# Optimization experiments

Hardware: AMD Instinct MI355X
Metric: run time of the kernel (lower is better)

## Reference

```python
import jax, jax.numpy as jnp
import numpy as np

B, N, F_IN, H, L, C = 64, 512, 21, 64, 3, 9
NEG_INF = -jnp.inf


def setup_inputs() -> dict:
    key = jax.random.key(0)
    ks = jax.random.split(key, 24)
    s = lambda shape, k, scale=0.05: jax.random.normal(ks[k], shape, dtype=jnp.float32) * scale
    return {
        "node_features": jax.random.normal(ks[0], (B, N, F_IN), dtype=jnp.float32),
        "adjacency": jax.random.bernoulli(ks[1], 0.05, (B, N, N)).astype(jnp.float32),
        "node_mask": jnp.ones((B, N), dtype=bool),
        "We": s((F_IN, H), 2), "be": jnp.zeros((H,), jnp.float32),
        "Wl": s((L, H, H), 3), "a_src": s((L, H), 4), "a_dst": s((L, H), 5),
        "gamma": jnp.ones((L, H), jnp.float32), "beta": jnp.zeros((L, H), jnp.float32),
        "P1": s((H, H), 6), "pb1": jnp.zeros((H,), jnp.float32),
        "P2": s((H,), 7), "pb2": jnp.zeros((), jnp.float32),
        "C1": s((H, H), 8), "cb1": jnp.zeros((H,), jnp.float32),
        "C2": s((H, C), 9), "cb2": jnp.zeros((C,), jnp.float32),
    }


def _layernorm(x, g, b, eps=1e-5):
    mu = x.mean(-1, keepdims=True)
    var = ((x - mu) ** 2).mean(-1, keepdims=True)
    return (x - mu) * jax.lax.rsqrt(var + eps) * g + b


def reference(node_features, adjacency, node_mask, We, be, Wl, a_src, a_dst,
              gamma, beta, P1, pb1, P2, pb2, C1, cb1, C2, cb2):
    # node embedding (dropout = identity in eval)
    h = jax.nn.relu(node_features @ We + be)  # [B,N,H]
    adj_zero = adjacency == 0
    for l in range(L):
        hW = h @ Wl[l]                                  # [B,N,H]
        attn = hW @ a_src[l]                            # [B,N] src scores
        attn = attn[:, :, None] + (hW @ a_dst[l])[:, None, :]  # [B,N,N]
        attn = jax.nn.leaky_relu(attn, 0.2)
        attn = jnp.where(adj_zero, NEG_INF, attn)
        attn = jnp.nan_to_num(jax.nn.softmax(attn, axis=-1), nan=0.0)
        h = _layernorm(h + attn @ hW, gamma[l], beta[l])
    # attention pooling
    pa = jnp.tanh(h @ P1 + pb1) @ P2 + pb2              # [B,N]
    pa = jnp.where(node_mask, pa, NEG_INF)
    pa = jnp.nan_to_num(jax.nn.softmax(pa, axis=-1), nan=0.0)
    g = jnp.einsum('bn,bnh->bh', pa, h)                 # [B,H]
    return jax.nn.relu(g @ C1 + cb1) @ C2 + cb2         # [B,C]
```

## Files before the change

kernel.cpp:

```cpp
#include <hip/hip_runtime.h>
#include <hip/hip_bf16.h>


#define WS_H     0
#define WS_HWA   2097152
#define WS_HWB   4194304
#define WS_SA    6291456
#define WS_TA    6324224
#define WS_SB    6356992
#define WS_TB    6389760
#define WS_PA    6422528
#define WS_DEG   6455296
#define WS_LIST_BYTES 25952256

__device__ __forceinline__ float wsum(float v) {
#pragma unroll
  for (int o = 32; o; o >>= 1) v += __shfl_xor(v, o, 64);
  return v;
}
__device__ __forceinline__ float wmax(float v) {
#pragma unroll
  for (int o = 32; o; o >>= 1) v = fmaxf(v, __shfl_xor(v, o, 64));
  return v;
}
__device__ __forceinline__ float rsum16(float v) {
#pragma unroll
  for (int o = 1; o < 16; o <<= 1) v += __shfl_xor(v, o, 64);
  return v;
}

__device__ __forceinline__ int row_base64(int blk) {
  int xcd = blk & 7;
  int i = blk >> 3;
  int batch = xcd * 8 + (i & 7);
  int sub = i >> 3;
  return batch * 512 + sub * 64;
}

template <int MODE>
__device__ __forceinline__ void gemm_tail(
    const float* lhT, const float* lw, int base, int tid,
    const float* __restrict__ v1, const float* __restrict__ v2,
    float* __restrict__ o1, float* __restrict__ o2, float* __restrict__ o3) {
  int tc = tid & 15, tr = tid >> 4;
  float acc[2][4] = {};
#pragma unroll 4
  for (int c = 0; c < 64; ++c) {
    float2 a = *(const float2*)&lhT[c * 68 + tr * 2];
    float4 bb = *(const float4*)&lw[c * 68 + tc * 4];
    float av[2] = {a.x, a.y};
    float bv[4] = {bb.x, bb.y, bb.z, bb.w};
#pragma unroll
    for (int i = 0; i < 2; ++i)
#pragma unroll
      for (int j = 0; j < 4; ++j) acc[i][j] = fmaf(av[i], bv[j], acc[i][j]);
  }
  float p1[4], p2[4];
#pragma unroll
  for (int j = 0; j < 4; ++j) { p1[j] = v1[tc * 4 + j]; p2[j] = v2[tc * 4 + j]; }
#pragma unroll
  for (int i = 0; i < 2; ++i) {
    int row = base + tr * 2 + i;
    if (MODE == 0) {
      *(float4*)&o1[(size_t)row * 64 + tc * 4] =
          make_float4(acc[i][0], acc[i][1], acc[i][2], acc[i][3]);
      float ps = acc[i][0] * p1[0] + acc[i][1] * p1[1] +
                 acc[i][2] * p1[2] + acc[i][3] * p1[3];
      float pt = acc[i][0] * p2[0] + acc[i][1] * p2[1] +
                 acc[i][2] * p2[2] + acc[i][3] * p2[3];
      ps = rsum16(ps);
      pt = rsum16(pt);
      if (tc == 0) { o2[row] = ps; o3[row] = pt; }
    } else {
      float p = 0.0f;
#pragma unroll
      for (int j = 0; j < 4; ++j) p += tanhf(acc[i][j] + p1[j]) * p2[j];
      p = rsum16(p);
      if (tc == 0) o2[row] = p;
    }
  }
}

__global__ __launch_bounds__(512) void k_embed_hw(
    const float* __restrict__ x, const float* __restrict__ We,
    const float* __restrict__ be, const float* __restrict__ adj,
    const float* __restrict__ W0, const float* __restrict__ asrc,
    const float* __restrict__ adst,
    float* __restrict__ h, int* __restrict__ deg,
    unsigned short* __restrict__ nlist,
    float* __restrict__ hW, float* __restrict__ s, float* __restrict__ t) {
  __shared__ float lhT[64 * 68];
  __shared__ float lw[64 * 68];
  int tid = threadIdx.x, lane = tid & 63, wv = tid >> 6;
  int base = row_base64(blockIdx.x);
#pragma unroll
  for (int i = 0; i < 2; ++i) {
    int k = tid + 512 * i;
    int rr = k >> 4, q = k & 15;
    *(float4*)&lw[rr * 68 + q * 4] = *(const float4*)&W0[rr * 64 + q * 4];
  }
  float wreg[21];
#pragma unroll
  for (int f = 0; f < 21; ++f) wreg[f] = We[f * 64 + lane];
  float bev = be[lane];
  unsigned long long lmask = (1ull << lane) - 1ull;
  int rb = base + wv * 8;
  for (int r = 0; r < 8; ++r) {
    int row = rb + r;
    const float4* ar = (const float4*)(adj + (size_t)row * 512);
    float4 a0 = ar[lane];
    float4 a1 = ar[64 + lane];
    const float* xr = x + (size_t)row * 21;
    float acc = bev;
#pragma unroll
    for (int f = 0; f < 21; ++f) acc = fmaf(xr[f], wreg[f], acc);
    acc = fmaxf(acc, 0.0f);
    h[(size_t)row * 64 + lane] = acc;
    lhT[lane * 68 + (row - base)] = acc;
    float comp[8] = {a0.x, a0.y, a0.z, a0.w, a1.x, a1.y, a1.z, a1.w};
    int cnt = 0;
#pragma unroll
    for (int c = 0; c < 8; ++c) {
      bool on = comp[c] != 0.0f;
      unsigned long long m = __ballot(on);
      if (on) {
        int pos = cnt + __popcll(m & lmask);
        int col = (c < 4) ? (lane * 4 + c) : (256 + lane * 4 + (c - 4));
        if (pos < 64)
          nlist[(size_t)row * 64 + pos] = (unsigned short)col;
      }
      cnt += __popcll(m);
    }
    if (lane == 0) deg[row] = cnt < 64 ? cnt : 64;
  }
  __syncthreads();
  gemm_tail<0>(lhT, lw, base, tid, asrc, adst, hW, s, t);
}

template <int MODE>
__global__ __launch_bounds__(512) void k_layer(
    float* __restrict__ h, const float* __restrict__ hWin,
    const float* __restrict__ sIn, const float* __restrict__ tIn,
    const int* __restrict__ deg, const unsigned short* __restrict__ nlist,
    const float* __restrict__ gamma, const float* __restrict__ beta,
    const float* __restrict__ Wn, const float* __restrict__ v1,
    const float* __restrict__ v2,
    float* __restrict__ hWout, float* __restrict__ sOut,
    float* __restrict__ tOut) {
  __shared__ float lhT[64 * 68];
  __shared__ float lw[64 * 68];
  __shared__ unsigned short lidx[8][64];
  __shared__ float lwgt[8][64];
  int tid = threadIdx.x, lane = tid & 63, wv = tid >> 6;
  int base = row_base64(blockIdx.x);
#pragma unroll
  for (int i = 0; i < 2; ++i) {
    int k = tid + 512 * i;
    int rr = k >> 4, q = k & 15;
    *(float4*)&lw[rr * 68 + q * 4] = *(const float4*)&Wn[rr * 64 + q * 4];
  }
  float gm = gamma[lane], bt = beta[lane];
  int b = base >> 9;
  const float* hWb = hWin + ((size_t)b << 9) * 64;
  const float* tb = tIn + ((size_t)b << 9);
  int rb = base + wv * 8;
  for (int r = 0; r < 8; ++r) {
    int row = rb + r;
    int dg = deg[row];
    float si = sIn[row];
    unsigned short jv = nlist[(size_t)row * 64 + lane];
    bool act = lane < dg;
    float tv = act ? tb[jv] : -INFINITY;
    float tmax = wmax(tv);
    float me = si + tmax;
    me = me > 0.0f ? me : 0.2f * me;
    float e = si + tv;
    e = e > 0.0f ? e : 0.2f * e;
    float wj = act ? __expf(e - me) : 0.0f;
    float dsum = wsum(wj);
    lidx[wv][lane] = jv;
    lwgt[wv][lane] = wj;
    float acc0 = 0.0f, acc1 = 0.0f;
    int n = 0;
    for (; n + 8 <= dg; n += 8) {
      float h0 = hWb[(size_t)lidx[wv][n + 0] * 64 + lane];
      float h1 = hWb[(size_t)lidx[wv][n + 1] * 64 + lane];
      float h2 = hWb[(size_t)lidx[wv][n + 2] * 64 + lane];
      float h3 = hWb[(size_t)lidx[wv][n + 3] * 64 + lane];
      float h4 = hWb[(size_t)lidx[wv][n + 4] * 64 + lane];
      float h5 = hWb[(size_t)lidx[wv][n + 5] * 64 + lane];
      float h6 = hWb[(size_t)lidx[wv][n + 6] * 64 + lane];
      float h7 = hWb[(size_t)lidx[wv][n + 7] * 64 + lane];
      acc0 = fmaf(lwgt[wv][n + 0], h0, acc0);
      acc1 = fmaf(lwgt[wv][n + 1], h1, acc1);
      acc0 = fmaf(lwgt[wv][n + 2], h2, acc0);
      acc1 = fmaf(lwgt[wv][n + 3], h3, acc1);
      acc0 = fmaf(lwgt[wv][n + 4], h4, acc0);
      acc1 = fmaf(lwgt[wv][n + 5], h5, acc1);
      acc0 = fmaf(lwgt[wv][n + 6], h6, acc0);
      acc1 = fmaf(lwgt[wv][n + 7], h7, acc1);
    }
    for (; n < dg; ++n)
      acc0 = fmaf(lwgt[wv][n], hWb[(size_t)lidx[wv][n] * 64 + lane], acc0);
    float acc = acc0 + acc1;
    float a = dg > 0 ? acc * (1.0f / dsum) : 0.0f;
    float xv = h[(size_t)row * 64 + lane] + a;
    float mu = wsum(xv) * 0.015625f;
    float dd = xv - mu;
    float var = wsum(dd * dd) * 0.015625f;
    float hn = fmaf(dd * rsqrtf(var + 1e-5f), gm, bt);
    h[(size_t)row * 64 + lane] = hn;
    lhT[lane * 68 + (row - base)] = hn;
  }
  __syncthreads();
  gemm_tail<MODE>(lhT, lw, base, tid, v1, v2, hWout, sOut, tOut);
}

__global__ __launch_bounds__(512) void k_pool(const float* __restrict__ h,
    const float* __restrict__ pa, const float* __restrict__ C1,
    const float* __restrict__ cb1, const float* __restrict__ C2,
    const float* __restrict__ cb2, float* __restrict__ out) {
  __shared__ float red[8];
  __shared__ float gpart[8][64];
  __shared__ float gl[64], rl[64];
  int b = ((blockIdx.x & 7) << 3) | (blockIdx.x >> 3);
  int tid = threadIdx.x, lane = tid & 63, wv = tid >> 6;
  float v = pa[b * 512 + tid];
  float m = wmax(v);
  if (lane == 0) red[wv] = m;
  __syncthreads();
  float bm = red[0];
#pragma unroll
  for (int w = 1; w < 8; ++w) bm = fmaxf(bm, red[w]);
  float e = __expf(v - bm);
  float sm = wsum(e);
  __syncthreads();
  if (lane == 0) red[wv] = sm;
  __syncthreads();
  float bs = 0.0f;
#pragma unroll
  for (int w = 0; w < 8; ++w) bs += red[w];
  float p = e / bs;
  const float* hb = h + ((size_t)b * 512) * 64;
  float g = 0.0f;
#pragma unroll
  for (int l = 0; l < 64; ++l) {
    float pj = __shfl(p, l, 64);
    g = fmaf(pj, hb[(size_t)(wv * 64 + l) * 64 + lane], g);
  }
  gpart[wv][lane] = g;
  __syncthreads();
  if (wv == 0) {
    float gg = 0.0f;
#pragma unroll
    for (int w = 0; w < 8; ++w) gg += gpart[w][lane];
    gl[lane] = gg;
    float rr = cb1[lane];
#pragma unroll
    for (int j = 0; j < 64; ++j) rr = fmaf(gl[j], C1[j * 64 + lane], rr);
    rr = fmaxf(rr, 0.0f);
    rl[lane] = rr;
    if (lane < 9) {
      float o = cb2[lane];
#pragma unroll
      for (int k = 0; k < 64; ++k) o = fmaf(rl[k], C2[k * 9 + lane], o);
      out[b * 9 + lane] = o;
    }
  }
}

extern "C" void kernel_launch(void* const* d_in, const int* in_sizes, int n_in,
                              void* d_out, int out_size, void* d_ws, size_t ws_size,
                              hipStream_t stream) {
  const float* x    = (const float*)d_in[0];
  const float* adj  = (const float*)d_in[1];
  const float* We   = (const float*)d_in[3];
  const float* be   = (const float*)d_in[4];
  const float* Wl   = (const float*)d_in[5];
  const float* asrc = (const float*)d_in[6];
  const float* adst = (const float*)d_in[7];
  const float* gamma= (const float*)d_in[8];
  const float* beta = (const float*)d_in[9];
  const float* P1   = (const float*)d_in[10];
  const float* pb1  = (const float*)d_in[11];
  const float* P2   = (const float*)d_in[12];
  const float* C1   = (const float*)d_in[14];
  const float* cb1  = (const float*)d_in[15];
  const float* C2   = (const float*)d_in[16];
  const float* cb2  = (const float*)d_in[17];
  float* out = (float*)d_out;

  float* ws  = (float*)d_ws;
  float* h   = ws + WS_H;
  float* hwA = ws + WS_HWA;
  float* hwB = ws + WS_HWB;
  float* sA  = ws + WS_SA;
  float* tA  = ws + WS_TA;
  float* sB  = ws + WS_SB;
  float* tB  = ws + WS_TB;
  float* pa  = ws + WS_PA;
  int*   deg = (int*)(ws + WS_DEG);
  unsigned short* nlist = (unsigned short*)((char*)d_ws + WS_LIST_BYTES);

  k_embed_hw<<<512, 512, 0, stream>>>(x, We, be, adj, Wl, asrc, adst,
                                      h, deg, nlist, hwA, sA, tA);
  k_layer<0><<<512, 512, 0, stream>>>(h, hwA, sA, tA, deg, nlist,
                                      gamma, beta, Wl + 4096,
                                      asrc + 64, adst + 64, hwB, sB, tB);
  k_layer<0><<<512, 512, 0, stream>>>(h, hwB, sB, tB, deg, nlist,
                                      gamma + 64, beta + 64, Wl + 8192,
                                      asrc + 128, adst + 128, hwA, sA, tA);
  k_layer<1><<<512, 512, 0, stream>>>(h, hwA, sA, tA, deg, nlist,
                                      gamma + 128, beta + 128, P1, pb1, P2,
                                      nullptr, pa, nullptr);
  k_pool<<<64, 512, 0, stream>>>(h, pa, C1, cb1, C2, cb2, out);
}
```

Measured before the change: 249.7 us.

## Stage per-batch hW into LDS and gather neighbors with readlane in layer kernel

Measured after the change: 236.5 us. 1.06x faster.

```diff
diff --git a/kernel.cpp b/kernel.cpp
--- a/kernel.cpp
+++ b/kernel.cpp
@@ -13,6 +13,9 @@
 #define WS_DEG   6455296
 #define WS_LIST_BYTES 25952256
 
+typedef const __attribute__((address_space(1))) unsigned int gu32;
+typedef __attribute__((address_space(3))) unsigned int lu32;
+
 __device__ __forceinline__ float wsum(float v) {
 #pragma unroll
   for (int o = 32; o; o >>= 1) v += __shfl_xor(v, o, 64);
@@ -27,6 +30,10 @@
 #pragma unroll
   for (int o = 1; o < 16; o <<= 1) v += __shfl_xor(v, o, 64);
   return v;
+}
+
+__device__ __forceinline__ void gl_lds16(const float* g, float* l) {
+  __builtin_amdgcn_global_load_lds((gu32*)g, (lu32*)l, 16, 0, 0);
 }
 
 __device__ __forceinline__ int row_base64(int blk) {
@@ -37,7 +44,7 @@
   return batch * 512 + sub * 64;
 }
 
-template <int MODE>
+template <int MODE, int LSTR>
 __device__ __forceinline__ void gemm_tail(
     const float* lhT, const float* lw, int base, int tid,
     const float* __restrict__ v1, const float* __restrict__ v2,
@@ -46,7 +53,7 @@
   float acc[2][4] = {};
 #pragma unroll 4
   for (int c = 0; c < 64; ++c) {
-    float2 a = *(const float2*)&lhT[c * 68 + tr * 2];
+    float2 a = *(const float2*)&lhT[c * LSTR + tr * 2];
     float4 bb = *(const float4*)&lw[c * 68 + tc * 4];
     float av[2] = {a.x, a.y};
     float bv[4] = {bb.x, bb.y, bb.z, bb.w};
@@ -134,11 +141,11 @@
     if (lane == 0) deg[row] = cnt < 64 ? cnt : 64;
   }
   __syncthreads();
-  gemm_tail<0>(lhT, lw, base, tid, asrc, adst, hW, s, t);
+  gemm_tail<0, 68>(lhT, lw, base, tid, asrc, adst, hW, s, t);
 }
 
 template <int MODE>
-__global__ __launch_bounds__(512) void k_layer(
+__global__ __launch_bounds__(1024) void k_layer(
     float* __restrict__ h, const float* __restrict__ hWin,
     const float* __restrict__ sIn, const float* __restrict__ tIn,
     const int* __restrict__ deg, const unsigned short* __restrict__ nlist,
@@ -147,73 +154,87 @@
     const float* __restrict__ v2,
     float* __restrict__ hWout, float* __restrict__ sOut,
     float* __restrict__ tOut) {
-  __shared__ float lhT[64 * 68];
+  __shared__ float hlds[512 * 64];
   __shared__ float lw[64 * 68];
-  __shared__ unsigned short lidx[8][64];
-  __shared__ float lwgt[8][64];
+  __shared__ float tlds[512];
   int tid = threadIdx.x, lane = tid & 63, wv = tid >> 6;
-  int base = row_base64(blockIdx.x);
-#pragma unroll
-  for (int i = 0; i < 2; ++i) {
-    int k = tid + 512 * i;
-    int rr = k >> 4, q = k & 15;
-    *(float4*)&lw[rr * 68 + q * 4] = *(const float4*)&Wn[rr * 64 + q * 4];
-  }
-  float gm = gamma[lane], bt = beta[lane];
-  int b = base >> 9;
-  const float* hWb = hWin + ((size_t)b << 9) * 64;
-  const float* tb = tIn + ((size_t)b << 9);
+  int xcd = blockIdx.x & 7;
+  int i = blockIdx.x >> 3;
+  int b = xcd * 8 + (i & 7);
+  int sub = i >> 3;
+  int base = b * 512 + sub * 128;
   int rb = base + wv * 8;
+
+  unsigned short jr[8]; float sir[8], hrr[8]; int dgr[8];
+#pragma unroll
   for (int r = 0; r < 8; ++r) {
     int row = rb + r;
-    int dg = deg[row];
-    float si = sIn[row];
-    unsigned short jv = nlist[(size_t)row * 64 + lane];
+    jr[r] = nlist[(size_t)row * 64 + lane];
+    sir[r] = sIn[row];
+    hrr[r] = h[(size_t)row * 64 + lane];
+    dgr[r] = deg[row];
+  }
+  {
+    int rr = tid >> 4, q = tid & 15;
+    *(float4*)&lw[rr * 68 + q * 4] = *(const float4*)&Wn[rr * 64 + q * 4];
+  }
+  const float* tb = tIn + ((size_t)b << 9);
+  if (tid < 128) *(float4*)&tlds[tid * 4] = *(const float4*)&tb[tid * 4];
+  {
+    const char* src = (const char*)(hWin + ((size_t)b << 9) * 64);
+    char* dst = (char*)hlds;
+#pragma unroll
+    for (int c = 0; c < 8; ++c) {
+      int off = wv * 8192 + c * 1024;
+      gl_lds16((const float*)(src + off + lane * 16), (float*)(dst + off));
+    }
+  }
+  __syncthreads();
+
+  float gm = gamma[lane], bt = beta[lane];
+  int jm[8]; float tvr[8];
+#pragma unroll
+  for (int r = 0; r < 8; ++r) {
+    jm[r] = (lane < dgr[r]) ? (int)jr[r] : 0;
+    tvr[r] = tlds[jm[r]];
+  }
+  float hst[8];
+#pragma unroll
+  for (int r = 0; r < 8; ++r) {
+    int dg = dgr[r];
     bool act = lane < dg;
-    float tv = act ? tb[jv] : -INFINITY;
-    float tmax = wmax(tv);
-    float me = si + tmax;
-    me = me > 0.0f ? me : 0.2f * me;
-    float e = si + tv;
+    float e = sir[r] + tvr[r];
     e = e > 0.0f ? e : 0.2f * e;
-    float wj = act ? __expf(e - me) : 0.0f;
+    float wj = act ? __expf(e) : 0.0f;
     float dsum = wsum(wj);
-    lidx[wv][lane] = jv;
-    lwgt[wv][lane] = wj;
     float acc0 = 0.0f, acc1 = 0.0f;
-    int n = 0;
-    for (; n + 8 <= dg; n += 8) {
-      float h0 = hWb[(size_t)lidx[wv][n + 0] * 64 + lane];
-      float h1 = hWb[(size_t)lidx[wv][n + 1] * 64 + lane];
-      float h2 = hWb[(size_t)lidx[wv][n + 2] * 64 + lane];
-      float h3 = hWb[(size_t)lidx[wv][n + 3] * 64 + lane];
-      float h4 = hWb[(size_t)lidx[wv][n + 4] * 64 + lane];
-      float h5 = hWb[(size_t)lidx[wv][n + 5] * 64 + lane];
-      float h6 = hWb[(size_t)lidx[wv][n + 6] * 64 + lane];
-      float h7 = hWb[(size_t)lidx[wv][n + 7] * 64 + lane];
-      acc0 = fmaf(lwgt[wv][n + 0], h0, acc0);
-      acc1 = fmaf(lwgt[wv][n + 1], h1, acc1);
-      acc0 = fmaf(lwgt[wv][n + 2], h2, acc0);
-      acc1 = fmaf(lwgt[wv][n + 3], h3, acc1);
-      acc0 = fmaf(lwgt[wv][n + 4], h4, acc0);
-      acc1 = fmaf(lwgt[wv][n + 5], h5, acc1);
-      acc0 = fmaf(lwgt[wv][n + 6], h6, acc0);
-      acc1 = fmaf(lwgt[wv][n + 7], h7, acc1);
-    }
-    for (; n < dg; ++n)
-      acc0 = fmaf(lwgt[wv][n], hWb[(size_t)lidx[wv][n] * 64 + lane], acc0);
-    float acc = acc0 + acc1;
-    float a = dg > 0 ? acc * (1.0f / dsum) : 0.0f;
-    float xv = h[(size_t)row * 64 + lane] + a;
-    float mu = wsum(xv) * 0.015625f;
-    float dd = xv - mu;
-    float var = wsum(dd * dd) * 0.015625f;
-    float hn = fmaf(dd * rsqrtf(var + 1e-5f), gm, bt);
-    h[(size_t)row * 64 + lane] = hn;
-    lhT[lane * 68 + (row - base)] = hn;
-  }
-  __syncthreads();
-  gemm_tail<MODE>(lhT, lw, base, tid, v1, v2, hWout, sOut, tOut);
+    int dg8 = (dg + 7) & ~7;
+    for (int n = 0; n < dg8; n += 8) {
+#pragma unroll
+      for (int k = 0; k < 8; k += 2) {
+        int j0 = __builtin_amdgcn_readlane(jm[r], n + k);
+        unsigned w0 = __builtin_amdgcn_readlane(__float_as_uint(wj), n + k);
+        int j1 = __builtin_amdgcn_readlane(jm[r], n + k + 1);
+        unsigned w1 = __builtin_amdgcn_readlane(__float_as_uint(wj), n + k + 1);
+        acc0 = fmaf(__uint_as_float(w0), hlds[j0 * 64 + lane], acc0);
+        acc1 = fmaf(__uint_as_float(w1), hlds[j1 * 64 + lane], acc1);
+      }
+    }
+    float a = dg > 0 ? (acc0 + acc1) * (1.0f / dsum) : 0.0f;
+    float xv = hrr[r] + a;
+    float s1 = wsum(xv), s2 = wsum(xv * xv);
+    float mu = s1 * 0.015625f;
+    float var = fmaf(-mu, mu, s2 * 0.015625f);
+    float hn = fmaf((xv - mu) * rsqrtf(var + 1e-5f), gm, bt);
+    h[(size_t)(rb + r) * 64 + lane] = hn;
+    hst[r] = hn;
+  }
+  __syncthreads();
+  float* lhT = hlds;
+#pragma unroll
+  for (int r = 0; r < 8; ++r) lhT[lane * 132 + (wv * 8 + r)] = hst[r];
+  __syncthreads();
+  gemm_tail<MODE, 132>(lhT, lw, base, tid, v1, v2, hWout, sOut, tOut);
 }
 
 __global__ __launch_bounds__(512) void k_pool(const float* __restrict__ h,
@@ -304,14 +325,14 @@
 
   k_embed_hw<<<512, 512, 0, stream>>>(x, We, be, adj, Wl, asrc, adst,
                                       h, deg, nlist, hwA, sA, tA);
-  k_layer<0><<<512, 512, 0, stream>>>(h, hwA, sA, tA, deg, nlist,
-                                      gamma, beta, Wl + 4096,
-                                      asrc + 64, adst + 64, hwB, sB, tB);
-  k_layer<0><<<512, 512, 0, stream>>>(h, hwB, sB, tB, deg, nlist,
-                                      gamma + 64, beta + 64, Wl + 8192,
-                                      asrc + 128, adst + 128, hwA, sA, tA);
-  k_layer<1><<<512, 512, 0, stream>>>(h, hwA, sA, tA, deg, nlist,
-                                      gamma + 128, beta + 128, P1, pb1, P2,
-                                      nullptr, pa, nullptr);
+  k_layer<0><<<256, 1024, 0, stream>>>(h, hwA, sA, tA, deg, nlist,
+                                       gamma, beta, Wl + 4096,
+                                       asrc + 64, adst + 64, hwB, sB, tB);
+  k_layer<0><<<256, 1024, 0, stream>>>(h, hwB, sB, tB, deg, nlist,
+                                       gamma + 64, beta + 64, Wl + 8192,
+                                       asrc + 128, adst + 128, hwA, sA, tA);
+  k_layer<1><<<256, 1024, 0, stream>>>(h, hwA, sA, tA, deg, nlist,
+                                       gamma + 128, beta + 128, P1, pb1, P2,
+                                       nullptr, pa, nullptr);
   k_pool<<<64, 512, 0, stream>>>(h, pa, C1, cb1, C2, cb2, out);
 }
```
